# Performance work log

Hardware: AMD Instinct MI355X
Metric: run time of the kernel (lower is better)

The kernel has to match this reference:

```python
import jax, jax.numpy as jnp
import numpy as np

N_STATE = 64
N_LAYERS = 4
D_MODEL = 512
D_OUT = 256
BATCH = 16
SEQLEN = 2048


def setup_inputs() -> dict:
    key = jax.random.key(0)
    ks = jax.random.split(key, 16)
    H, N, nl = D_MODEL, N_STATE, N_LAYERS
    inp = {}
    inp["x"] = jax.random.normal(ks[0], (BATCH, SEQLEN, D_MODEL), dtype=jnp.float32)
    # encoder / decoder dense
    inp["enc_w"] = jax.random.normal(ks[1], (D_MODEL, D_MODEL), jnp.float32) / np.sqrt(D_MODEL)
    inp["enc_b"] = jnp.zeros((D_MODEL,), jnp.float32)
    inp["dec_w"] = jax.random.normal(ks[2], (D_MODEL, D_OUT), jnp.float32) / np.sqrt(D_MODEL)
    inp["dec_b"] = jnp.zeros((D_OUT,), jnp.float32)
    # per-layer LayerNorm
    inp["ln_scale"] = jnp.ones((nl, D_MODEL), jnp.float32)
    inp["ln_bias"] = jnp.zeros((nl, D_MODEL), jnp.float32)
    # per-layer S4 DPLR params (stored as real/imag float pairs)
    inp["lambda_re"] = -0.5 * jnp.ones((nl, H, N), jnp.float32)
    inp["lambda_im"] = jnp.broadcast_to(np.pi * jnp.arange(N, dtype=jnp.float32), (nl, H, N))
    inp["p_re"] = jax.random.normal(ks[3], (nl, H, N), jnp.float32) * 0.5
    inp["p_im"] = jax.random.normal(ks[4], (nl, H, N), jnp.float32) * 0.5
    inp["b_re"] = jax.random.normal(ks[5], (nl, H, N), jnp.float32) * 0.5
    inp["b_im"] = jax.random.normal(ks[6], (nl, H, N), jnp.float32) * 0.5
    inp["c_re"] = jax.random.normal(ks[7], (nl, H, N), jnp.float32) * 0.5
    inp["c_im"] = jax.random.normal(ks[8], (nl, H, N), jnp.float32) * 0.5
    inp["log_step"] = jax.random.uniform(ks[9], (nl, H), jnp.float32, minval=np.log(1e-3), maxval=np.log(1e-1))
    inp["d_param"] = jnp.ones((nl, H), jnp.float32)
    # per-layer output Dense
    inp["out_w"] = jax.random.normal(ks[10], (nl, D_MODEL, D_MODEL), jnp.float32) / np.sqrt(D_MODEL)
    inp["out_b"] = jnp.zeros((nl, D_MODEL), jnp.float32)
    return inp


def _layer_norm(x, scale, bias, eps=1e-6):
    mu = jnp.mean(x, axis=-1, keepdims=True)
    var = jnp.mean(jnp.square(x - mu), axis=-1, keepdims=True)
    return (x - mu) * jax.lax.rsqrt(var + eps) * scale + bias


def _kernel_dplr(Lam, P, B, C, step, L):
    # Lam,P,B,C: [H,N] complex64; step: [H] float32 -> K: [H,L] float32
    theta = (2.0 * np.pi / L) * jnp.arange(L, dtype=jnp.float32)
    Omega = jnp.exp(-1j * theta)                        # [L] roots of unity
    g = (2.0 / step)[:, None] * ((1.0 - Omega) / (1.0 + Omega))[None, :]  # [H,L]
    c = 2.0 / (1.0 + Omega)                             # [L]
    r = 1.0 / (g[:, :, None] - Lam[:, None, :])         # [H,L,N] resolvent (Cauchy)
    Cc, Pc = jnp.conj(C), jnp.conj(P)
    k00 = jnp.einsum("hn,hln->hl", Cc * B, r)
    k01 = jnp.einsum("hn,hln->hl", Cc * P, r)
    k10 = jnp.einsum("hn,hln->hl", Pc * B, r)
    k11 = jnp.einsum("hn,hln->hl", Pc * P, r)
    at_roots = c[None, :] * (k00 - k01 * (1.0 / (1.0 + k11)) * k10)  # [H,L]
    return jnp.fft.ifft(at_roots, n=L, axis=-1).real


def _s4_apply(u, Lam, P, B, C, step, D):
    # u: [Bt,L,H]; causal FFT convolution with kernel K[h,:] per channel
    L = u.shape[1]
    K = _kernel_dplr(Lam, P, B, C, step, L)             # [H,L]
    ud = jnp.fft.rfft(u, n=2 * L, axis=1)               # [Bt,L+1,H]
    Kd = jnp.fft.rfft(K, n=2 * L, axis=-1)              # [H,L+1]
    y = jnp.fft.irfft(ud * Kd.T[None], n=2 * L, axis=1)[:, :L]
    return y + D[None, None, :] * u


def reference(x, enc_w, enc_b, ln_scale, ln_bias, lambda_re, lambda_im,
              p_re, p_im, b_re, b_im, c_re, c_im, log_step, d_param,
              out_w, out_b, dec_w, dec_b):
    h = x @ enc_w + enc_b
    n_layers = ln_scale.shape[0]
    for i in range(n_layers):
        skip = h
        z = _layer_norm(h, ln_scale[i], ln_bias[i])
        Lam = lambda_re[i] + 1j * lambda_im[i]
        P = p_re[i] + 1j * p_im[i]
        B = b_re[i] + 1j * b_im[i]
        C = c_re[i] + 1j * c_im[i]
        z = _s4_apply(z, Lam, P, B, C, jnp.exp(log_step[i]), d_param[i])
        z = jax.nn.gelu(z)
        z = z @ out_w[i] + out_b[i]
        h = skip + z  # dropout=0.0 -> identity
    logits = h @ dec_w + dec_b
    return jax.nn.log_softmax(logits, axis=-1)
```

## Files before the change

kernel.cpp:

```cpp
#include <hip/hip_runtime.h>
#include <hip/hip_bf16.h>

#define NLAY 4
#define DH   512
#define NST  64
#define NB   16
#define SL   2048
#define NDO  256
#define BL   (NB*SL)
#define KDIM 512
#define TWOPI 6.283185307179586476925287

typedef unsigned short u16;
typedef __attribute__((ext_vector_type(8))) short  short8v;
typedef __attribute__((ext_vector_type(8))) unsigned short ushort8v;
typedef __attribute__((ext_vector_type(4))) float  f32x4;

#define RCPF(x) __builtin_amdgcn_rcpf(x)

__device__ __forceinline__ float bf2f(u16 v){
  union { unsigned u; float f; } x; x.u = ((unsigned)v) << 16; return x.f;
}
__device__ __forceinline__ u16 f2bf(float f){
  union { float f; unsigned u; } x; x.f = f;
  unsigned u = x.u;
  unsigned r = u + 0x7fffu + ((u >> 16) & 1u);
  return (u16)(r >> 16);
}
__device__ __forceinline__ void cmulw(float& xr, float& xi, float wr, float wi){
  float tr = xr*wr - xi*wi;
  xi = fmaf(xr, wi, xi*wr);
  xr = tr;
}
__device__ __forceinline__ float gelu_fast(float v){
  const float c0 = 0.7978845608028654f;
  float u = c0 * fmaf(0.044715f, v*v*v, v);
  return v * RCPF(1.0f + __expf(-2.0f * u));
}
__device__ __forceinline__ void gload16(const void* g, void* l){
  __builtin_amdgcn_global_load_lds(
      (__attribute__((address_space(1))) void*)(g),
      (__attribute__((address_space(3))) void*)(l), 16, 0, 0);
}

template<int SGN>
__device__ __forceinline__ void dft4w(float& r0, float& i0, float& r1, float& i1,
                                      float& r2, float& i2, float& r3, float& i3){
  const float t0r = r0 + r2, t0i = i0 + i2;
  const float t1r = r0 - r2, t1i = i0 - i2;
  const float t2r = r1 + r3, t2i = i1 + i3;
  const float t3r = r1 - r3, t3i = i1 - i3;
  r0 = t0r + t2r; i0 = t0i + t2i;
  r2 = t0r - t2r; i2 = t0i - t2i;
  if (SGN < 0){ r1 = t1r + t3i; i1 = t1i - t3r; r3 = t1r - t3i; i3 = t1i + t3r; }
  else        { r1 = t1r - t3i; i1 = t1i + t3r; r3 = t1r + t3i; i3 = t1i - t3r; }
}

template<int SGN>
__device__ __forceinline__ void dft16(float* re, float* im){
#pragma unroll
  for (int b = 0; b < 4; b++)
    dft4w<SGN>(re[b], im[b], re[4+b], im[4+b], re[8+b], im[8+b], re[12+b], im[12+b]);
  const float C1 = 0.92387953251128675613f, S1_ = 0.38268343236508977172f;
  const float C2 = 0.70710678118654752440f;
  const float sg = (SGN < 0) ? -1.f : 1.f;
  cmulw(re[5],  im[5],   C1,  sg*S1_);
  cmulw(re[9],  im[9],   C2,  sg*C2);
  cmulw(re[13], im[13],  S1_, sg*C1);
  cmulw(re[6],  im[6],   C2,  sg*C2);
  cmulw(re[10], im[10],  0.f, sg*1.f);
  cmulw(re[14], im[14], -C2,  sg*C2);
  cmulw(re[7],  im[7],   S1_, sg*C1);
  cmulw(re[11], im[11], -C2,  sg*C2);
  cmulw(re[15], im[15], -C1,  sg*(-S1_));
#pragma unroll
  for (int c = 0; c < 4; c++)
    dft4w<SGN>(re[4*c], im[4*c], re[4*c+1], im[4*c+1], re[4*c+2], im[4*c+2], re[4*c+3], im[4*c+3]);
  float tr_, ti_;
#define SWP(A,B) tr_=re[A]; re[A]=re[B]; re[B]=tr_; ti_=im[A]; im[A]=im[B]; im[B]=ti_;
  SWP(1,4) SWP(2,8) SWP(3,12) SWP(6,9) SWP(7,13) SWP(11,14)
#undef SWP
}

__device__ __forceinline__ int cxpad(int i){ return i + (i >> 4) + ((i >> 8) << 1); }
#define CXSZ 4384

__device__ __forceinline__ void fwd4096(float* re, float* im, float2* cx, int t){
  dft16<-1>(re, im);
  const float a0 = -(float)(TWOPI/4096.0) * (float)t;
#pragma unroll
  for (int k = 0; k < 16; k++){
    if (k){ float sn = __sinf(a0*(float)k), cs = __cosf(a0*(float)k); cmulw(re[k], im[k], cs, sn); }
    cx[cxpad(t + 256*k)] = make_float2(re[k], im[k]);
  }
  __syncthreads();
  const int k1 = t >> 4, m2 = t & 15;
  const int b2 = k1*256 + m2;
#pragma unroll
  for (int j = 0; j < 16; j++){ float2 v = cx[cxpad(b2 + 16*j)]; re[j] = v.x; im[j] = v.y; }
  dft16<-1>(re, im);
  const float b0 = -(float)(TWOPI/256.0) * (float)m2;
  __syncthreads();
#pragma unroll
  for (int k = 0; k < 16; k++){
    if (k){ float sn = __sinf(b0*(float)k), cs = __cosf(b0*(float)k); cmulw(re[k], im[k], cs, sn); }
    cx[cxpad(b2 + 16*k)] = make_float2(re[k], im[k]);
  }
  __syncthreads();
#pragma unroll
  for (int j = 0; j < 16; j++){ float2 v = cx[cxpad(16*t + j)]; re[j] = v.x; im[j] = v.y; }
  dft16<-1>(re, im);
}

__device__ __forceinline__ void inv4096(float* re, float* im, float2* cx, int t){
  dft16<1>(re, im);
#pragma unroll
  for (int j = 0; j < 16; j++) cx[cxpad(16*t + j)] = make_float2(re[j], im[j]);
  __syncthreads();
  const int k1 = t >> 4, m2 = t & 15;
  const int b2 = k1*256 + m2;
  const float b0 = (float)(TWOPI/256.0) * (float)m2;
#pragma unroll
  for (int k = 0; k < 16; k++){
    float2 v = cx[cxpad(b2 + 16*k)];
    re[k] = v.x; im[k] = v.y;
    if (k){ float sn = __sinf(b0*(float)k), cs = __cosf(b0*(float)k); cmulw(re[k], im[k], cs, sn); }
  }
  dft16<1>(re, im);
  __syncthreads();
#pragma unroll
  for (int j = 0; j < 16; j++) cx[cxpad(b2 + 16*j)] = make_float2(re[j], im[j]);
  __syncthreads();
  const float a0 = (float)(TWOPI/4096.0) * (float)t;
#pragma unroll
  for (int k = 0; k < 16; k++){
    float2 v = cx[cxpad(t + 256*k)];
    re[k] = v.x; im[k] = v.y;
    if (k){ float sn = __sinf(a0*(float)k), cs = __cosf(a0*(float)k); cmulw(re[k], im[k], cs, sn); }
  }
  dft16<1>(re, im);
}

__global__ __launch_bounds__(256) void prep_k(
  const float* __restrict__ lam_re, const float* __restrict__ lam_im,
  const float* __restrict__ p_re,  const float* __restrict__ p_im,
  const float* __restrict__ b_re,  const float* __restrict__ b_im,
  const float* __restrict__ c_re,  const float* __restrict__ c_im,
  float4* __restrict__ cwA, float4* __restrict__ cwB, float* __restrict__ cwS)
{
  const int i = blockIdx.x * 256 + threadIdx.x;
  const float lr = lam_re[i], li = lam_im[i];
  const float pr = p_re[i],  pi = p_im[i];
  const float br = b_re[i],  bi = b_im[i];
  const float cr = c_re[i],  ci = c_im[i];
  cwA[i] = make_float4(lr, li, cr*br + ci*bi, cr*bi - ci*br);
  cwB[i] = make_float4(cr*pr + ci*pi, cr*pi - ci*pr, pr*br + pi*bi, pr*bi - pi*br);
  cwS[i] = pr*pr + pi*pi;
}

__global__ __launch_bounds__(256) void cauchy_k(
    const float4* __restrict__ cwA, const float4* __restrict__ cwB,
    const float* __restrict__ cwS, const float* __restrict__ lstep,
    float2* __restrict__ Kd)
{
  const int t = threadIdx.x;
  const int h = blockIdx.y, lay = blockIdx.z;
  const int lb = blockIdx.x * 256 + t;
  const int wb = (lay*DH + h) * NST;
  const float tw0 = 2.0f * expf(-lstep[lay*DH + h]);

  float T0,T1, g0,g1;
  { float sn, cs;
    sincosf((float)(TWOPI/4096.0)*(float)(lb       ), &sn, &cs); T0 = sn*RCPF(cs); g0 = tw0*T0;
    sincosf((float)(TWOPI/4096.0)*(float)(lb + 1024), &sn, &cs); T1 = sn*RCPF(cs); g1 = tw0*T1;
  }

  float k00r0=0,k00i0=0,k01r0=0,k01i0=0,k10r0=0,k10i0=0,k11r0=0,k11i0=0;
  float k00r1=0,k00i1=0,k01r1=0,k01i1=0,k10r1=0,k10i1=0,k11r1=0,k11i1=0;

#pragma unroll 2
  for (int n = 0; n < NST; n++){
    const float4 A  = cwA[wb + n];
    const float4 Bv = cwB[wb + n];
    const float w11 = cwS[wb + n];
    const float nlr = -A.x;
    const float dr2 = A.x * A.x;
#define CSTEP(J) { \
    const float di = g##J - A.y; \
    const float sI = RCPF(fmaf(di, di, dr2)); \
    const float ivr = nlr * sI, ivi = -di * sI; \
    k00r##J = fmaf(A.z,  ivr, fmaf(-A.w,  ivi, k00r##J)); \
    k00i##J = fmaf(A.z,  ivi, fmaf( A.w,  ivr, k00i##J)); \
    k01r##J = fmaf(Bv.x, ivr, fmaf(-Bv.y, ivi, k01r##J)); \
    k01i##J = fmaf(Bv.x, ivi, fmaf( Bv.y, ivr, k01i##J)); \
    k10r##J = fmaf(Bv.z, ivr, fmaf(-Bv.w, ivi, k10r##J)); \
    k10i##J = fmaf(Bv.z, ivi, fmaf( Bv.w, ivr, k10i##J)); \
    k11r##J = fmaf(w11,  ivr, k11r##J); \
    k11i##J = fmaf(w11,  ivi, k11i##J); }
    CSTEP(0) CSTEP(1)
#undef CSTEP
  }

  float2* kp = Kd + (size_t)(lay*DH + h) * 4096;
#define COUT(J, LOFF) { \
    const float d1r = 1.f + k11r##J, d1i = k11i##J; \
    const float idn = RCPF(fmaf(d1r, d1r, d1i*d1i)); \
    const float wr = k01r##J*k10r##J - k01i##J*k10i##J; \
    const float wi = k01r##J*k10i##J + k01i##J*k10r##J; \
    const float vr = fmaf(wr, d1r,  wi*d1i) * idn; \
    const float vi = fmaf(wi, d1r, -wr*d1i) * idn; \
    const float sr = k00r##J - vr, si = k00i##J - vi; \
    kp[lb + LOFF] = make_float2(fmaf(-T##J, si, sr), fmaf(T##J, sr, si)); }
  COUT(0, 0) COUT(1, 1024)
#undef COUT
}

__global__ __launch_bounds__(256) void kdfft_k(float2* __restrict__ Kd){
  __shared__ float  ar[SL], ai[SL];
  __shared__ float2 cx[CXSZ];
  const int t = threadIdx.x;
  const size_t base = (size_t)blockIdx.x * 4096;
#pragma unroll
  for (int q = 0; q < 8; q++){
    const int l = t + 256*q;
    float2 v = Kd[base + l];
    const int brv = __brev((unsigned)l) >> 21;
    ar[brv] = v.x; ai[brv] = v.y;
  }
  __syncthreads();

  for (int s = 0; s < 11; s++){
    const int half = 1 << s;
    const float fac = (float)(TWOPI) / (float)(2 << s);
#pragma unroll
    for (int q = 0; q < 4; q++){
      const int v = t + 256*q;
      const int pos = v & (half - 1);
      const int i0 = ((v >> s) << (s+1)) + pos;
      const int i1 = i0 + half;
      const float ang = fac * (float)pos;
      const float wc = __cosf(ang), ws = __sinf(ang);
      const float xr = ar[i1], xi = ai[i1];
      const float tr = wc*xr - ws*xi, ti = fmaf(wc, xi, ws*xr);
      const float ur_ = ar[i0], ui_ = ai[i0];
      ar[i0] = ur_ + tr; ai[i0] = ui_ + ti;
      ar[i1] = ur_ - tr; ai[i1] = ui_ - ti;
    }
    __syncthreads();
  }

  float re[16], im[16];
#pragma unroll
  for (int j = 0; j < 16; j++){
    re[j] = (j < 8) ? ar[t + 256*j] * (1.0f/2048.f) : 0.f;
    im[j] = 0.f;
  }
  fwd4096(re, im, cx, t);
  float2* kp = Kd + base + 16*t;
#pragma unroll
  for (int k = 0; k < 16; k += 2)
    *(float4*)(kp + k) = make_float4(re[k], im[k], re[k+1], im[k+1]);
}

__global__ __launch_bounds__(256) void wconv_k(const float* __restrict__ src,
    u16* __restrict__ dst, int K, int N){
  __shared__ u16 tile[64][72];
  const size_t mb = (size_t)blockIdx.z * K * N;
  const int k0 = blockIdx.x * 64, n0 = blockIdx.y * 64;
  const int r = threadIdx.x >> 2, c4 = (threadIdx.x & 3) * 16;
  const float* s = src + mb + (size_t)(k0 + r) * N + n0 + c4;
  float4 f0 = *(const float4*)s, f1 = *(const float4*)(s+4);
  float4 f2 = *(const float4*)(s+8), f3 = *(const float4*)(s+12);
  tile[c4+0][r]=f2bf(f0.x); tile[c4+1][r]=f2bf(f0.y); tile[c4+2][r]=f2bf(f0.z); tile[c4+3][r]=f2bf(f0.w);
  tile[c4+4][r]=f2bf(f1.x); tile[c4+5][r]=f2bf(f1.y); tile[c4+6][r]=f2bf(f1.z); tile[c4+7][r]=f2bf(f1.w);
  tile[c4+8][r]=f2bf(f2.x); tile[c4+9][r]=f2bf(f2.y); tile[c4+10][r]=f2bf(f2.z); tile[c4+11][r]=f2bf(f2.w);
  tile[c4+12][r]=f2bf(f3.x); tile[c4+13][r]=f2bf(f3.y); tile[c4+14][r]=f2bf(f3.z); tile[c4+15][r]=f2bf(f3.w);
  __syncthreads();
  u16* d = dst + mb + (size_t)(n0 + r) * K + k0 + c4;
  *(ushort8v*)d       = *(const ushort8v*)&tile[r][c4];
  *(ushort8v*)(d + 8) = *(const ushort8v*)&tile[r][c4 + 8];
}

#define LTILE 32
__device__ __forceinline__ int lnswz(int h){ return ((h >> 1) + (h >> 6)) & 3; }

__global__ __launch_bounds__(256) void lnt_k(const u16* __restrict__ hsrc,
    const float* __restrict__ gam, const float* __restrict__ bet,
    u16* __restrict__ zT){
  __shared__ u16 tile[DH][LTILE];
  __shared__ float smu[LTILE], srs[LTILE];
  const int t = threadIdx.x;
  const int b = blockIdx.y, l0 = blockIdx.x * LTILE;
  const int r = t >> 3, hb = (t & 7) * 64;
  const u16* p = hsrc + ((size_t)b * SL + l0 + r) * DH + hb;
  float s = 0.f, sq = 0.f;
#pragma unroll
  for (int j8 = 0; j8 < 8; j8++){
    ushort8v w = *(const ushort8v*)(p + j8*8);
    const int h0 = hb + j8*8;
#pragma unroll
    for (int d = 0; d < 8; d++){
      const float f = bf2f((u16)w[d]);
      s += f; sq = fmaf(f, f, sq);
      tile[h0+d][r ^ (lnswz(h0+d) << 3)] = (u16)w[d];
    }
  }
  s  += __shfl_xor(s, 1);  sq += __shfl_xor(sq, 1);
  s  += __shfl_xor(s, 2);  sq += __shfl_xor(sq, 2);
  s  += __shfl_xor(s, 4);  sq += __shfl_xor(sq, 4);
  if ((t & 7) == 0){
    const float mu = s * (1.0f/DH);
    smu[r] = mu;
    srs[r] = rsqrtf(sq * (1.0f/DH) - mu*mu + 1e-6f);
  }
  __syncthreads();

#pragma unroll
  for (int hh = 0; hh < 2; hh++){
    const int h = t + hh*256;
    const float g = gam[h], be = bet[h];
    const int sw = lnswz(h);
    u16* dst = zT + ((size_t)b * DH + h) * SL + l0;
#pragma unroll
    for (int og = 0; og < 4; og++){
      const int lg = og ^ sw;
      ushort8v v = *(const ushort8v*)&tile[h][og*8];
      const float4 m0 = *(const float4*)&smu[lg*8];
      const float4 m1 = *(const float4*)&smu[lg*8 + 4];
      const float4 r0 = *(const float4*)&srs[lg*8];
      const float4 r1 = *(const float4*)&srs[lg*8 + 4];
      ushort8v o;
      o[0] = f2bf(fmaf(bf2f((u16)v[0]) - m0.x, r0.x*g, be));
      o[1] = f2bf(fmaf(bf2f((u16)v[1]) - m0.y, r0.y*g, be));
      o[2] = f2bf(fmaf(bf2f((u16)v[2]) - m0.z, r0.z*g, be));
      o[3] = f2bf(fmaf(bf2f((u16)v[3]) - m0.w, r0.w*g, be));
      o[4] = f2bf(fmaf(bf2f((u16)v[4]) - m1.x, r1.x*g, be));
      o[5] = f2bf(fmaf(bf2f((u16)v[5]) - m1.y, r1.y*g, be));
      o[6] = f2bf(fmaf(bf2f((u16)v[6]) - m1.z, r1.z*g, be));
      o[7] = f2bf(fmaf(bf2f((u16)v[7]) - m1.w, r1.w*g, be));
      *(ushort8v*)(dst + lg*8) = o;
    }
  }
}

__global__ __launch_bounds__(256) void s4conv_k(
    const u16* __restrict__ zT, const float2* __restrict__ Kd,
    const float* __restrict__ dpar, u16* __restrict__ yT)
{
  __shared__ float2 cx[CXSZ];
  const int t = threadIdx.x;
  const int wg = blockIdx.x;
  const int h = wg & 511, bp = wg >> 9;
  const u16* r1 = zT + ((size_t)(2*bp) * DH + h) * SL;
  const u16* r2 = r1 + (size_t)DH * SL;
  float ur1[8], ur2[8];
  float re[16], im[16];
#pragma unroll
  for (int j = 0; j < 8; j++){
    ur1[j] = bf2f(r1[t + 256*j]);
    ur2[j] = bf2f(r2[t + 256*j]);
    re[j] = ur1[j]; im[j] = ur2[j];
  }
#pragma unroll
  for (int j = 8; j < 16; j++){ re[j] = 0.f; im[j] = 0.f; }

  fwd4096(re, im, cx, t);

  const float2* kp = Kd + (size_t)h * 4096 + 16*t;
#pragma unroll
  for (int k = 0; k < 16; k += 2){
    float4 w2 = *(const float4*)(kp + k);
    cmulw(re[k],   im[k],   w2.x, w2.y);
    cmulw(re[k+1], im[k+1], w2.z, w2.w);
  }

  inv4096(re, im, cx, t);

  const float Dv = dpar[h];
  u16* y1 = yT + ((size_t)(2*bp) * DH + h) * SL;
  u16* y2 = y1 + (size_t)DH * SL;
#pragma unroll
  for (int j = 0; j < 8; j++){
    float v1 = fmaf(re[j], (1.0f/4096.f), Dv * ur1[j]);
    float v2 = fmaf(im[j], (1.0f/4096.f), Dv * ur2[j]);
    y1[t + 256*j] = f2bf(gelu_fast(v1));
    y2[t + 256*j] = f2bf(gelu_fast(v2));
  }
}

__global__ __launch_bounds__(256) void gemm_at_k(
    const u16* __restrict__ A, const u16* __restrict__ Wt,
    const float* __restrict__ bias,
    const u16* __restrict__ resid, u16* __restrict__ Cout,
    int Mb, int N)
{
  __shared__ u16 As[128][40];
  __shared__ u16 Bs[128][40];
  const int t = threadIdx.x;
  const int n0 = blockIdx.x * 128, m0 = blockIdx.y * 128, bb = blockIdx.z;
  const int lane = t & 63, wv = t >> 6;
  const int wm = (wv >> 1) * 64, wn = (wv & 1) * 64;
  f32x4 acc[4][4];
#pragma unroll
  for (int mi = 0; mi < 4; mi++)
#pragma unroll
    for (int ni = 0; ni < 4; ni++) acc[mi][ni] = {0.f, 0.f, 0.f, 0.f};

  const size_t Abase = (size_t)bb * KDIM * Mb;

  for (int k0 = 0; k0 < KDIM; k0 += 32){
    __syncthreads();
    {
      const int kk = t >> 3, ch = t & 7;
      const u16* srca = A + Abase + (size_t)(k0 + kk) * Mb + m0 + ch*16;
      ushort8v v0 = *(const ushort8v*)srca;
      ushort8v v1 = *(const ushort8v*)(srca + 8);
      const int col = (kk & 7) | (((kk >> 3) ^ (ch & 3)) << 3);
#pragma unroll
      for (int i = 0; i < 8; i++){
        As[ch*16 + i][col]     = (u16)v0[i];
        As[ch*16 + 8 + i][col] = (u16)v1[i];
      }
    }
    {
      const int r = t >> 1, kh = (t & 1) << 4;
      const u16* srcb = Wt + (size_t)(n0 + r) * KDIM + k0 + kh;
      ushort8v v0 = *(const ushort8v*)srcb;
      ushort8v v1 = *(const ushort8v*)(srcb + 8);
      const int s3 = (r >> 4) & 3;
      const int c0 = (((kh >> 3) ^ s3) << 3);
      const int c1 = ((((kh >> 3) + 1) ^ s3) << 3);
      *(ushort8v*)&Bs[r][c0] = v0;
      *(ushort8v*)&Bs[r][c1] = v1;
    }
    __syncthreads();

    const int ko = (lane >> 4) * 8;
    const int fr = lane & 15;
    short8v af[4], bf[4];
#pragma unroll
    for (int mi = 0; mi < 4; mi++){
      const int col = (((ko >> 3) ^ (((wm >> 4) + mi) & 3)) << 3);
      af[mi] = *(const short8v*)&As[wm + mi*16 + fr][col];
    }
#pragma unroll
    for (int ni = 0; ni < 4; ni++){
      const int col = (((ko >> 3) ^ (((wn >> 4) + ni) & 3)) << 3);
      bf[ni] = *(const short8v*)&Bs[wn + ni*16 + fr][col];
    }
#pragma unroll
    for (int mi = 0; mi < 4; mi++)
#pragma unroll
      for (int ni = 0; ni < 4; ni++)
        acc[mi][ni] = __builtin_amdgcn_mfma_f32_16x16x32_bf16(af[mi], bf[ni], acc[mi][ni], 0, 0, 0);
  }

  const int fr = lane & 15;
  const int rq = (lane >> 4) * 4;
#pragma unroll
  for (int mi = 0; mi < 4; mi++){
#pragma unroll
    for (int ni = 0; ni < 4; ni++){
      const int gn = n0 + wn + ni*16 + fr;
      const float bs = bias[gn];
#pragma unroll
      for (int q = 0; q < 4; q++){
        const int gm = m0 + wm + mi*16 + rq + q;
        const size_t idx = ((size_t)bb * Mb + gm) * N + gn;
        Cout[idx] = f2bf(acc[mi][ni][q] + bs + bf2f(resid[idx]));
      }
    }
  }
}

template<int AMODE, bool OUTBF>
__global__ __launch_bounds__(256) void gemm_k(
    const void* __restrict__ Aptr, const u16* __restrict__ Wt,
    const float* __restrict__ bias, void* __restrict__ Coutv,
    int Mb, int N)
{
  __shared__ u16 As[4096];
  __shared__ u16 Bs[4096];
  const int t = threadIdx.x;
  const int n0 = blockIdx.x * 128, m0 = blockIdx.y * 128;
  const int lane = t & 63, wv = t >> 6;
  const int wm = (wv >> 1) * 64, wn = (wv & 1) * 64;
  const int wbase = t & 192;
  f32x4 acc[4][4];
#pragma unroll
  for (int mi = 0; mi < 4; mi++)
#pragma unroll
    for (int ni = 0; ni < 4; ni++) acc[mi][ni] = {0.f, 0.f, 0.f, 0.f};

  const u16*  Ab = (const u16*)Aptr;
  const float* Af = (const float*)Aptr;

  for (int k0 = 0; k0 < KDIM; k0 += 32){
    __syncthreads();
    if (AMODE == 0){
#pragma unroll
      for (int i = 0; i < 2; i++){
        const int G = i*256 + t;
        const int r = G >> 2;
        const int g = ((G & 3) ^ r ^ (r >> 2)) & 3;
        gload16(Ab + (size_t)(m0 + r) * KDIM + k0 + g*8,
                As + (size_t)(i*256 + wbase) * 8);
      }
    } else {
      const int r = t >> 1, kh = (t & 1) << 4;
      const float* sf = Af + (size_t)(m0 + r) * KDIM + k0 + kh;
      float4 f0 = *(const float4*)sf,     f1 = *(const float4*)(sf + 4);
      float4 f2 = *(const float4*)(sf+8), f3 = *(const float4*)(sf + 12);
      ushort8v v0, v1;
      v0[0]=f2bf(f0.x); v0[1]=f2bf(f0.y); v0[2]=f2bf(f0.z); v0[3]=f2bf(f0.w);
      v0[4]=f2bf(f1.x); v0[5]=f2bf(f1.y); v0[6]=f2bf(f1.z); v0[7]=f2bf(f1.w);
      v1[0]=f2bf(f2.x); v1[1]=f2bf(f2.y); v1[2]=f2bf(f2.z); v1[3]=f2bf(f2.w);
      v1[4]=f2bf(f3.x); v1[5]=f2bf(f3.y); v1[6]=f2bf(f3.z); v1[7]=f2bf(f3.w);
      const int key = (r ^ (r >> 2)) & 3;
      *(ushort8v*)&As[(size_t)((r<<2) | ((kh>>3) ^ key))*8]       = v0;
      *(ushort8v*)&As[(size_t)((r<<2) | (((kh>>3)+1) ^ key))*8]   = v1;
    }
#pragma unroll
    for (int i = 0; i < 2; i++){
      const int G = i*256 + t;
      const int r = G >> 2;
      const int g = ((G & 3) ^ r ^ (r >> 2)) & 3;
      gload16(Wt + (size_t)(n0 + r) * KDIM + k0 + g*8,
              Bs + (size_t)(i*256 + wbase) * 8);
    }
    __syncthreads();

    const int fr = lane & 15, g4 = lane >> 4;
    short8v af[4], bf[4];
#pragma unroll
    for (int mi = 0; mi < 4; mi++){
      const int r = wm + mi*16 + fr;
      af[mi] = *(const short8v*)&As[(size_t)((r<<2) | ((g4 ^ r ^ (r>>2)) & 3)) * 8];
    }
#pragma unroll
    for (int ni = 0; ni < 4; ni++){
      const int r = wn + ni*16 + fr;
      bf[ni] = *(const short8v*)&Bs[(size_t)((r<<2) | ((g4 ^ r ^ (r>>2)) & 3)) * 8];
    }
#pragma unroll
    for (int mi = 0; mi < 4; mi++)
#pragma unroll
      for (int ni = 0; ni < 4; ni++)
        acc[mi][ni] = __builtin_amdgcn_mfma_f32_16x16x32_bf16(af[mi], bf[ni], acc[mi][ni], 0, 0, 0);
  }

  const int fr = lane & 15;
  const int rq = (lane >> 4) * 4;
#pragma unroll
  for (int mi = 0; mi < 4; mi++){
#pragma unroll
    for (int ni = 0; ni < 4; ni++){
      const int gn = n0 + wn + ni*16 + fr;
      const float bs = bias[gn];
#pragma unroll
      for (int q = 0; q < 4; q++){
        const int gm = m0 + wm + mi*16 + rq + q;
        const size_t idx = (size_t)gm * N + gn;
        float v = acc[mi][ni][q] + bs;
        if (OUTBF) ((u16*)Coutv)[idx] = f2bf(v);
        else       ((float*)Coutv)[idx] = v;
      }
    }
  }
}

__global__ __launch_bounds__(256) void lsm_k(float* __restrict__ o){
  const int row = blockIdx.x * 4 + (threadIdx.x >> 6);
  const int lane = threadIdx.x & 63;
  float* p = o + (size_t)row * NDO + lane * 4;
  float4 v = *(const float4*)p;
  float mx = fmaxf(fmaxf(v.x, v.y), fmaxf(v.z, v.w));
#pragma unroll
  for (int q = 32; q; q >>= 1) mx = fmaxf(mx, __shfl_xor(mx, q));
  float e = __expf(v.x - mx) + __expf(v.y - mx) + __expf(v.z - mx) + __expf(v.w - mx);
#pragma unroll
  for (int q = 32; q; q >>= 1) e += __shfl_xor(e, q);
  const float lse = mx + __logf(e);
  v.x -= lse; v.y -= lse; v.z -= lse; v.w -= lse;
  *(float4*)p = v;
}

extern "C" void kernel_launch(void* const* d_in, const int* in_sizes, int n_in,
                              void* d_out, int out_size, void* d_ws, size_t ws_size,
                              hipStream_t stream)
{
  (void)in_sizes; (void)n_in; (void)out_size; (void)ws_size;
  const float* x      = (const float*)d_in[0];
  const float* enc_w  = (const float*)d_in[1];
  const float* enc_b  = (const float*)d_in[2];
  const float* dec_w  = (const float*)d_in[3];
  const float* dec_b  = (const float*)d_in[4];
  const float* ln_s   = (const float*)d_in[5];
  const float* ln_b   = (const float*)d_in[6];
  const float* lam_re = (const float*)d_in[7];
  const float* lam_im = (const float*)d_in[8];
  const float* p_re   = (const float*)d_in[9];
  const float* p_im   = (const float*)d_in[10];
  const float* b_re   = (const float*)d_in[11];
  const float* b_im   = (const float*)d_in[12];
  const float* c_re   = (const float*)d_in[13];
  const float* c_im   = (const float*)d_in[14];
  const float* lstep  = (const float*)d_in[15];
  const float* d_par  = (const float*)d_in[16];
  const float* out_w  = (const float*)d_in[17];
  const float* out_b  = (const float*)d_in[18];

  char* ws = (char*)d_ws;
  u16*    hbuf = (u16*)(ws);
  u16*    zT   = (u16*)  (ws + (size_t)67108864 + 33554432);
  u16*    yT   = (u16*)  (ws + (size_t)67108864 + 2*33554432);
  float2* Kd   = (float2*)(ws + (size_t)67108864 + 3*33554432);
  u16*    Wt   = (u16*)  (ws + (size_t)67108864 + 3*33554432 + 67108864);
  u16*    WtEnc = Wt;
  u16*    WtOut = Wt + 262144;
  u16*    WtDec = Wt + 262144*5;
  float*  outp = (float*)d_out;

  float4* cwA = (float4*)d_out;
  float4* cwB = cwA + 131072;
  float*  cwS = (float*)(cwB + 131072);

  prep_k<<<dim3(NLAY*DH*NST/256), 256, 0, stream>>>(lam_re, lam_im, p_re, p_im,
                                                    b_re, b_im, c_re, c_im, cwA, cwB, cwS);
  wconv_k<<<dim3(8, 8, 1), 256, 0, stream>>>(enc_w, WtEnc, KDIM, DH);
  wconv_k<<<dim3(8, 8, NLAY), 256, 0, stream>>>(out_w, WtOut, KDIM, DH);
  wconv_k<<<dim3(8, 4, 1), 256, 0, stream>>>(dec_w, WtDec, KDIM, NDO);
  cauchy_k<<<dim3(4, DH, NLAY), 256, 0, stream>>>(cwA, cwB, cwS, lstep, Kd);
  kdfft_k<<<dim3(NLAY*DH), 256, 0, stream>>>(Kd);
  gemm_k<2,true><<<dim3(DH/128, BL/128, 1), 256, 0, stream>>>(
      x, WtEnc, enc_b, hbuf, BL, DH);
  for (int i = 0; i < NLAY; i++){
    lnt_k<<<dim3(SL/LTILE, NB), 256, 0, stream>>>(hbuf, ln_s + i*DH, ln_b + i*DH, zT);
    s4conv_k<<<dim3((NB/2)*DH), 256, 0, stream>>>(
        zT, Kd + (size_t)i*DH*4096, d_par + i*DH, yT);
    gemm_at_k<<<dim3(DH/128, SL/128, NB), 256, 0, stream>>>(
        yT, WtOut + (size_t)i*262144, out_b + i*DH, hbuf, hbuf, SL, DH);
  }
  gemm_k<0,false><<<dim3(NDO/128, BL/128, 1), 256, 0, stream>>>(
      hbuf, WtDec, dec_b, outp, BL, NDO);
  lsm_k<<<dim3(BL/4), 256, 0, stream>>>(outp);
}
```

Before: 765.9 us.

## Use direct global-to-LDS loads and transposing LDS reads in A-transposed GEMM

Operand tiles in the A-transposed GEMM are now staged with direct global-to-LDS 16-byte loads (gload16). The old path went through registers, and the A tile was scattered into LDS with many 2-byte stores. A is stored in its k-major layout and transposed on the way out using ds_read_b64_tr_b16, and B uses an XOR-swizzled packed layout. The intent is to remove the costly scalar transpose stores and register staging. It depends on the correctness of the new layout and swizzle mapping and on inline asm with manual waitcnt.

```diff
diff --git a/kernel.cpp b/kernel.cpp
--- a/kernel.cpp
+++ b/kernel.cpp
@@ -15,6 +15,7 @@
 typedef __attribute__((ext_vector_type(8))) short  short8v;
 typedef __attribute__((ext_vector_type(8))) unsigned short ushort8v;
 typedef __attribute__((ext_vector_type(4))) float  f32x4;
+typedef __attribute__((ext_vector_type(2))) unsigned int uint2v;
 
 #define RCPF(x) __builtin_amdgcn_rcpf(x)
 
@@ -394,59 +395,71 @@
     const u16* __restrict__ resid, u16* __restrict__ Cout,
     int Mb, int N)
 {
-  __shared__ u16 As[128][40];
-  __shared__ u16 Bs[128][40];
+  __shared__ u16 As[4096];
+  __shared__ u16 Bs[4096];
   const int t = threadIdx.x;
   const int n0 = blockIdx.x * 128, m0 = blockIdx.y * 128, bb = blockIdx.z;
   const int lane = t & 63, wv = t >> 6;
   const int wm = (wv >> 1) * 64, wn = (wv & 1) * 64;
+  const int wbase = t & 192;
   f32x4 acc[4][4];
 #pragma unroll
   for (int mi = 0; mi < 4; mi++)
 #pragma unroll
     for (int ni = 0; ni < 4; ni++) acc[mi][ni] = {0.f, 0.f, 0.f, 0.f};
 
-  const size_t Abase = (size_t)bb * KDIM * Mb;
+  int kA[2], mA[2];
+#pragma unroll
+  for (int i = 0; i < 2; i++){
+    const int G = i*256 + t;
+    const int s = G >> 3, r8 = G & 7;
+    const int q = s & 7;
+    const int kb = ((q & 3) << 1) | (q >> 2);
+    kA[i] = kb*4 + (r8 >> 1);
+    mA[i] = (s >> 3)*16 + (r8 & 1)*8;
+  }
+  const size_t Abase = (size_t)bb * DH * (size_t)Mb;
+  const unsigned lds_as =
+      (unsigned)(unsigned long long)(__attribute__((address_space(3))) u16*)As;
 
   for (int k0 = 0; k0 < KDIM; k0 += 32){
     __syncthreads();
-    {
-      const int kk = t >> 3, ch = t & 7;
-      const u16* srca = A + Abase + (size_t)(k0 + kk) * Mb + m0 + ch*16;
-      ushort8v v0 = *(const ushort8v*)srca;
-      ushort8v v1 = *(const ushort8v*)(srca + 8);
-      const int col = (kk & 7) | (((kk >> 3) ^ (ch & 3)) << 3);
-#pragma unroll
-      for (int i = 0; i < 8; i++){
-        As[ch*16 + i][col]     = (u16)v0[i];
-        As[ch*16 + 8 + i][col] = (u16)v1[i];
-      }
-    }
-    {
-      const int r = t >> 1, kh = (t & 1) << 4;
-      const u16* srcb = Wt + (size_t)(n0 + r) * KDIM + k0 + kh;
-      ushort8v v0 = *(const ushort8v*)srcb;
-      ushort8v v1 = *(const ushort8v*)(srcb + 8);
-      const int s3 = (r >> 4) & 3;
-      const int c0 = (((kh >> 3) ^ s3) << 3);
-      const int c1 = ((((kh >> 3) + 1) ^ s3) << 3);
-      *(ushort8v*)&Bs[r][c0] = v0;
-      *(ushort8v*)&Bs[r][c1] = v1;
+#pragma unroll
+    for (int i = 0; i < 2; i++)
+      gload16(A + Abase + (size_t)(k0 + kA[i]) * Mb + m0 + mA[i],
+              As + (size_t)(i*256 + wbase) * 8);
+#pragma unroll
+    for (int i = 0; i < 2; i++){
+      const int G = i*256 + t;
+      const int r = G >> 2;
+      const int g = ((G & 3) ^ r ^ (r >> 2)) & 3;
+      gload16(Wt + (size_t)(n0 + r) * KDIM + k0 + g*8,
+              Bs + (size_t)(i*256 + wbase) * 8);
     }
     __syncthreads();
 
-    const int ko = (lane >> 4) * 8;
-    const int fr = lane & 15;
+    uint2v ra[4], rb[4];
+#pragma unroll
+    for (int mi = 0; mi < 4; mi++){
+      const unsigned b = lds_as + (unsigned)(((wm >> 4) + mi) * 1024 + lane * 8);
+      asm volatile("ds_read_b64_tr_b16 %0, %1" : "=v"(ra[mi]) : "v"(b));
+      asm volatile("ds_read_b64_tr_b16 %0, %1 offset:512" : "=v"(rb[mi]) : "v"(b));
+    }
+    asm volatile("s_waitcnt lgkmcnt(0)" ::: "memory");
+    __builtin_amdgcn_sched_barrier(0);
+
     short8v af[4], bf[4];
 #pragma unroll
     for (int mi = 0; mi < 4; mi++){
-      const int col = (((ko >> 3) ^ (((wm >> 4) + mi) & 3)) << 3);
-      af[mi] = *(const short8v*)&As[wm + mi*16 + fr][col];
-    }
+      union { uint2v u2[2]; short8v s8; } cvt;
+      cvt.u2[0] = ra[mi]; cvt.u2[1] = rb[mi];
+      af[mi] = cvt.s8;
+    }
+    const int fr = lane & 15, g4 = lane >> 4;
 #pragma unroll
     for (int ni = 0; ni < 4; ni++){
-      const int col = (((ko >> 3) ^ (((wn >> 4) + ni) & 3)) << 3);
-      bf[ni] = *(const short8v*)&Bs[wn + ni*16 + fr][col];
+      const int r = wn + ni*16 + fr;
+      bf[ni] = *(const short8v*)&Bs[(size_t)((r<<2) | ((g4 ^ r ^ (r>>2)) & 3)) * 8];
     }
 #pragma unroll
     for (int mi = 0; mi < 4; mi++)
```

New measurement: 732.0 us. -4.4%, faster.
